# Kernel tuning notes

Measured on AMD Instinct MI355X. Metric: run time of the kernel, lower is better.

Reference implementation:

```python
import jax, jax.numpy as jnp
import numpy as np

N_NODES = 100_000
N_EDGES = 2_500_000
N_GRAPHS = 1000
F_IN, H, C = 4, 32, 3


def setup_inputs() -> dict:
    key = jax.random.key(0)
    ks = jax.random.split(key, 12)
    x = jax.random.normal(ks[0], (N_NODES, F_IN), dtype=jnp.float32)
    edge_index = jax.random.randint(ks[1], (2, N_EDGES), 0, N_NODES, dtype=jnp.int64)
    edge_weight = jax.random.uniform(ks[2], (N_EDGES,), dtype=jnp.float32)
    batch = jnp.sort(jax.random.randint(ks[3], (N_NODES,), 0, N_GRAPHS, dtype=jnp.int64))
    # GCNConv weights (glorot-ish) and biases
    W1 = jax.random.normal(ks[4], (F_IN, H), dtype=jnp.float32) * (1.0 / np.sqrt(F_IN))
    b1 = jnp.zeros((H,), dtype=jnp.float32)
    W2 = jax.random.normal(ks[5], (H, H), dtype=jnp.float32) * (1.0 / np.sqrt(H))
    b2 = jnp.zeros((H,), dtype=jnp.float32)
    W3 = jax.random.normal(ks[6], (H, H), dtype=jnp.float32) * (1.0 / np.sqrt(H))
    b3 = jnp.zeros((H,), dtype=jnp.float32)
    lin_w = jax.random.normal(ks[7], (H, C), dtype=jnp.float32) * (1.0 / np.sqrt(H))
    lin_b = jnp.zeros((C,), dtype=jnp.float32)
    return {"x": x, "edge_index": edge_index, "edge_weight": edge_weight, "batch": batch,
            "W1": W1, "b1": b1, "W2": W2, "b2": b2, "W3": W3, "b3": b3,
            "lin_w": lin_w, "lin_b": lin_b}


def _gcn_norm(edge_index, edge_weight, n_nodes):
    # PyG gcn_norm with add_self_loops=True: D^{-1/2} A_hat D^{-1/2}
    loop = jnp.arange(n_nodes, dtype=edge_index.dtype)
    row = jnp.concatenate([edge_index[0], loop])
    col = jnp.concatenate([edge_index[1], loop])
    w = jnp.concatenate([edge_weight, jnp.ones((n_nodes,), edge_weight.dtype)])
    deg = jax.ops.segment_sum(w, col, num_segments=n_nodes)
    dinv = jnp.where(deg > 0, jax.lax.rsqrt(jnp.where(deg > 0, deg, 1.0)), 0.0)
    norm = dinv[row] * w * dinv[col]
    return row, col, norm


def _gcn_conv(x, W, b, row, col, norm, n_nodes):
    h = x @ W                                  # [N, out]
    msg = norm[:, None] * h[row]               # gather + scale  [E+N, out]
    agg = jax.ops.segment_sum(msg, col, num_segments=n_nodes)
    return agg + b


def reference(x, edge_index, edge_weight, batch, W1, b1, W2, b2, W3, b3, lin_w, lin_b):
    n = x.shape[0]
    row, col, norm = _gcn_norm(edge_index, edge_weight, n)
    # dropout is identity in eval mode
    h = jax.nn.relu(_gcn_conv(x, W1, b1, row, col, norm, n))
    h = jax.nn.relu(_gcn_conv(h, W2, b2, row, col, norm, n))
    h = _gcn_conv(h, W3, b3, row, col, norm, n)
    # global_mean_pool over batch ids
    sums = jax.ops.segment_sum(h, batch, num_segments=N_GRAPHS)        # [G, H]
    cnt = jax.ops.segment_sum(jnp.ones((n,), h.dtype), batch, num_segments=N_GRAPHS)
    pooled = sums / jnp.maximum(cnt, 1.0)[:, None]
    return jax.nn.softmax(pooled @ lin_w + lin_b, axis=1)
```

## Files before the change

### kernel.cpp

```cpp
#include <hip/hip_runtime.h>
#include <hip/hip_fp16.h>

typedef unsigned long long ull;
typedef unsigned int uint;

#define BLOCK 256
#define CHUNK 8192
#define BN 128
#define PB 128
#define WINV (1.0f / 32768.0f)

__global__ void init_kernel(float* __restrict__ sums, float* __restrict__ cnt,
                            int* __restrict__ rowptr, int G, int nN, int nE) {
    int i = blockIdx.x * BLOCK + threadIdx.x;
    if (i < G * 32) sums[i] = 0.f;
    if (i < G) cnt[i] = 0.f;
    if (i == 0) rowptr[nN] = nE;
}

__global__ void p1_kernel(const int* __restrict__ col, int* __restrict__ cntmat,
                          int nE, int NBUK) {
    __shared__ int hist[1024];
    for (int i = threadIdx.x; i < NBUK; i += BLOCK) hist[i] = 0;
    __syncthreads();
    int base = blockIdx.x * CHUNK;
    int end = min(base + CHUNK, nE);
    for (int e = base + threadIdx.x; e < end; e += BLOCK)
        atomicAdd(&hist[col[e] >> 7], 1);
    __syncthreads();
    for (int i = threadIdx.x; i < NBUK; i += BLOCK)
        cntmat[(size_t)blockIdx.x * NBUK + i] = hist[i];
}

__global__ void p2a_kernel(int* __restrict__ cntmat, int* __restrict__ tot, int C, int NBUK) {
    int wv = threadIdx.x >> 6, lane = threadIdx.x & 63;
    int b = blockIdx.x * 4 + wv;
    if (b >= NBUK) return;
    int running = 0;
    for (int seg = 0; seg < C; seg += 64) {
        int c = seg + lane;
        int v = (c < C) ? cntmat[(size_t)c * NBUK + b] : 0;
        int s = v;
#pragma unroll
        for (int off = 1; off < 64; off <<= 1) {
            int u = __shfl_up(s, off);
            if (lane >= off) s += u;
        }
        if (c < C) cntmat[(size_t)c * NBUK + b] = running + (s - v);
        running += __shfl(s, 63);
    }
    if (lane == 0) tot[b] = running;
}

__global__ void p2b_kernel(const int* __restrict__ tot, int* __restrict__ bb, int NBUK, int nE) {
    __shared__ int s[1024];
    int t = threadIdx.x;
    int v = (t < NBUK) ? tot[t] : 0;
    s[t] = v;
    __syncthreads();
    for (int off = 1; off < 1024; off <<= 1) {
        int u = (t >= off) ? s[t - off] : 0;
        __syncthreads();
        s[t] += u;
        __syncthreads();
    }
    if (t < NBUK) bb[t] = s[t] - v;
    if (t == 0) bb[NBUK] = nE;
}

__global__ void p3_kernel(const int* __restrict__ row, const int* __restrict__ col,
                          const float* __restrict__ w, const int* __restrict__ cntmat,
                          const int* __restrict__ bb, ull* __restrict__ sorted,
                          int nE, int NBUK) {
    __shared__ int cur[1024];
    for (int i = threadIdx.x; i < NBUK; i += BLOCK)
        cur[i] = cntmat[(size_t)blockIdx.x * NBUK + i] + bb[i];
    __syncthreads();
    int base = blockIdx.x * CHUNK;
    int end = min(base + CHUNK, nE);
    for (int e = base + threadIdx.x; e < end; e += BLOCK) {
        int c = col[e], r = row[e];
        float ww = w[e];
        int b = c >> 7;
        int rk = atomicAdd(&cur[b], 1);
        ull ent = ((ull)(((uint)(c & 127) << 17) | (uint)r) << 32) | (ull)__float_as_uint(ww);
        sorted[rk] = ent;
    }
}

__global__ void p4_kernel(const ull* __restrict__ sorted, const int* __restrict__ bb,
                          float* __restrict__ dinv, int* __restrict__ rowptr,
                          uint* __restrict__ csr4, int nN) {
    __shared__ float wsum[BN];
    __shared__ int cntL[BN];
    __shared__ int scanS[BN];
    __shared__ int cur[BN];
    if (threadIdx.x < BN) { wsum[threadIdx.x] = 0.f; cntL[threadIdx.x] = 0; }
    __syncthreads();
    int b = blockIdx.x;
    int e0 = bb[b], e1 = bb[b + 1];
    for (int i = e0 + threadIdx.x; i < e1; i += BLOCK) {
        ull ent = sorted[i];
        int dl = (int)(ent >> 49) & 127;
        atomicAdd(&cntL[dl], 1);
        atomicAdd(&wsum[dl], __uint_as_float((uint)ent));
    }
    __syncthreads();
    if (threadIdx.x < BN) scanS[threadIdx.x] = cntL[threadIdx.x];
    __syncthreads();
    for (int off = 1; off < BN; off <<= 1) {
        int u = 0;
        if (threadIdx.x < BN && threadIdx.x >= off) u = scanS[threadIdx.x - off];
        __syncthreads();
        if (threadIdx.x < BN) scanS[threadIdx.x] += u;
        __syncthreads();
    }
    if (threadIdx.x < BN) {
        int n = b * BN + threadIdx.x;
        if (n < nN) {
            dinv[n] = rsqrtf(1.0f + wsum[threadIdx.x]);
            int rp = e0 + scanS[threadIdx.x] - cntL[threadIdx.x];
            rowptr[n] = rp;
            cur[threadIdx.x] = rp;
        }
    }
    __syncthreads();
    for (int i = e0 + threadIdx.x; i < e1; i += BLOCK) {
        ull ent = sorted[i];
        int dl = (int)(ent >> 49) & 127;
        uint src = (uint)(ent >> 32) & 0x1FFFFu;
        float ww = __uint_as_float((uint)ent);
        int wq = min((int)(ww * 32768.0f + 0.5f), 32767);
        int pos = atomicAdd(&cur[dl], 1);
        csr4[pos] = (src << 15) | (uint)wq;
    }
}

__global__ void ux_kernel(const float* __restrict__ x, const float* __restrict__ dinv,
                          float* __restrict__ u_x, int nN) {
    int i = blockIdx.x * BLOCK + threadIdx.x;
    if (i < nN * 4) u_x[i] = x[i] * dinv[i >> 2];
}

__global__ void layer1_pass(const float* __restrict__ u_x, const int* __restrict__ rowptr,
                            const uint* __restrict__ csr4, const float* __restrict__ dinv,
                            const float* __restrict__ W1, const float* __restrict__ b1,
                            const float* __restrict__ W2, __half* __restrict__ t_next, int nN) {
    __shared__ float W1s[4 * 32];
    __shared__ float W2s[32 * 32];
    __shared__ float b1s[32];
    __shared__ float hS[BLOCK / 64][32];
    if (threadIdx.x < 128) W1s[threadIdx.x] = W1[threadIdx.x];
    for (int i = threadIdx.x; i < 32 * 32; i += BLOCK) W2s[i] = W2[i];
    if (threadIdx.x < 32) b1s[threadIdx.x] = b1[threadIdx.x];
    __syncthreads();

    int wv = threadIdx.x >> 6, lane = threadIdx.x & 63;
    int n = blockIdx.x * (BLOCK / 64) + wv;
    if (n >= nN) return;

    int el = lane >> 2, comp = lane & 3;
    float di = dinv[n];
    int s0 = rowptr[n], s1 = rowptr[n + 1];
    float acc = (el == 0) ? u_x[(size_t)n * 4 + comp] : 0.0f;
    int j = s0;
    for (; j + 32 <= s1; j += 32) {
        uint ea = csr4[j + el], eb = csr4[j + 16 + el];
        acc = fmaf((float)(ea & 32767u) * WINV, u_x[(size_t)(ea >> 15) * 4 + comp], acc);
        acc = fmaf((float)(eb & 32767u) * WINV, u_x[(size_t)(eb >> 15) * 4 + comp], acc);
    }
    for (; j + 16 <= s1; j += 16) {
        uint e = csr4[j + el];
        acc = fmaf((float)(e & 32767u) * WINV, u_x[(size_t)(e >> 15) * 4 + comp], acc);
    }
    if (j + el < s1) {
        uint e = csr4[j + el];
        acc = fmaf((float)(e & 32767u) * WINV, u_x[(size_t)(e >> 15) * 4 + comp], acc);
    }
#pragma unroll
    for (int off = 4; off < 64; off <<= 1) acc += __shfl_xor(acc, off);
    float a0 = di * __shfl(acc, 0), a1 = di * __shfl(acc, 1);
    float a2c = di * __shfl(acc, 2), a3 = di * __shfl(acc, 3);

    int f = lane & 31, e2 = lane >> 5;
    float h = b1s[f];
    h = fmaf(a0, W1s[0 * 32 + f], h);
    h = fmaf(a1, W1s[1 * 32 + f], h);
    h = fmaf(a2c, W1s[2 * 32 + f], h);
    h = fmaf(a3, W1s[3 * 32 + f], h);
    h = fmaxf(h, 0.0f);
    if (lane < 32) hS[wv][f] = h;
    float o = 0.0f;
#pragma unroll
    for (int k = 0; k < 16; ++k) {
        int kk = e2 * 16 + k;
        o = fmaf(hS[wv][kk], W2s[kk * 32 + f], o);
    }
    o += __shfl_xor(o, 32);
    if (lane < 32) t_next[(size_t)n * 32 + f] = __float2half(di * o);
}

template <bool LAST>
__global__ void layer_pass(const __half* __restrict__ t, const int* __restrict__ rowptr,
                           const uint* __restrict__ csr4, const float* __restrict__ dinv,
                           const float* __restrict__ b, const float* __restrict__ W,
                           __half* __restrict__ t_next, __half* __restrict__ stage, int nN) {
    __shared__ float Ws[32 * 32];
    __shared__ float hS[BLOCK / 64][32];
    if (!LAST) {
        for (int i = threadIdx.x; i < 32 * 32; i += BLOCK) Ws[i] = W[i];
        __syncthreads();
    }
    int wv = threadIdx.x >> 6, lane = threadIdx.x & 63;
    int e2 = lane >> 5, f = lane & 31;
    int n = blockIdx.x * (BLOCK / 64) + wv;
    if (n >= nN) return;

    float di = dinv[n];
    int s0 = rowptr[n], s1 = rowptr[n + 1];
    float acc = (e2 == 0) ? __half2float(t[(size_t)n * 32 + f]) : 0.0f;

    int j4 = s0;
    for (; j4 + 16 <= s1; j4 += 16) {
        uint p[8]; float v[8];
#pragma unroll
        for (int u = 0; u < 8; ++u) p[u] = csr4[j4 + 2 * u + e2];
#pragma unroll
        for (int u = 0; u < 8; ++u) v[u] = __half2float(t[(size_t)(p[u] >> 15) * 32 + f]);
#pragma unroll
        for (int u = 0; u < 8; ++u) acc = fmaf((float)(p[u] & 32767u) * WINV, v[u], acc);
    }
    for (; j4 + 4 <= s1; j4 += 4) {
        uint p[2]; float v[2];
#pragma unroll
        for (int u = 0; u < 2; ++u) p[u] = csr4[j4 + 2 * u + e2];
#pragma unroll
        for (int u = 0; u < 2; ++u) v[u] = __half2float(t[(size_t)(p[u] >> 15) * 32 + f]);
#pragma unroll
        for (int u = 0; u < 2; ++u) acc = fmaf((float)(p[u] & 32767u) * WINV, v[u], acc);
    }
    for (int j = j4 + e2; j < s1; j += 2) {
        uint p = csr4[j];
        acc = fmaf((float)(p & 32767u) * WINV, __half2float(t[(size_t)(p >> 15) * 32 + f]), acc);
    }

    acc += __shfl_xor(acc, 32);
    float h = di * acc + b[f];

    if (LAST) {
        if (lane < 32) stage[(size_t)n * 32 + f] = __float2half(h);
    } else {
        h = fmaxf(h, 0.0f);
        if (lane < 32) hS[wv][f] = h;
        float o = 0.0f;
#pragma unroll
        for (int k = 0; k < 16; ++k) {
            int kk = e2 * 16 + k;
            o = fmaf(hS[wv][kk], Ws[kk * 32 + f], o);
        }
        o += __shfl_xor(o, 32);
        if (lane < 32) t_next[(size_t)n * 32 + f] = __float2half(di * o);
    }
}

__global__ void pool_kernel(const __half* __restrict__ stage, const int* __restrict__ batch,
                            float* __restrict__ sums, float* __restrict__ cnt, int nN) {
    __shared__ float accS[PB][32];
    __shared__ float cntS[PB];
    __shared__ int g0s;
    int n0 = blockIdx.x * PB;
    for (int i = threadIdx.x; i < PB * 32; i += BLOCK) ((float*)accS)[i] = 0.0f;
    for (int i = threadIdx.x; i < PB; i += BLOCK) cntS[i] = 0.0f;
    if (threadIdx.x == 0) g0s = batch[n0];
    __syncthreads();
    int g0 = g0s;
    int f = threadIdx.x & 31, sub = threadIdx.x >> 5;
    for (int k = 0; k < PB / 8; ++k) {
        int n = n0 + sub + k * 8;
        if (n < nN) {
            int g = batch[n];
            int off = g - g0;
            float v = __half2float(stage[(size_t)n * 32 + f]);
            if (off < PB) {
                atomicAdd(&accS[off][f], v);
                if (f == 0) atomicAdd(&cntS[off], 1.0f);
            } else {
                atomicAdd(&sums[(size_t)g * 32 + f], v);
                if (f == 0) atomicAdd(&cnt[g], 1.0f);
            }
        }
    }
    __syncthreads();
    int nLast = min(n0 + PB, nN) - 1;
    int range = min(batch[nLast] - g0, PB - 1);
    for (int s = sub; s <= range; s += 8) {
        atomicAdd(&sums[(size_t)(g0 + s) * 32 + f], accS[s][f]);
        if (f == 0) atomicAdd(&cnt[g0 + s], cntS[s]);
    }
}

__global__ void final_kernel(const float* __restrict__ sums, const float* __restrict__ cnt,
                             const float* __restrict__ lin_w, const float* __restrict__ lin_b,
                             float* __restrict__ out, int G) {
    int g = blockIdx.x * blockDim.x + threadIdx.x;
    if (g >= G) return;
    float c = fmaxf(cnt[g], 1.0f);
    float inv = 1.0f / c;
    float l0 = lin_b[0], l1 = lin_b[1], l2 = lin_b[2];
#pragma unroll
    for (int f = 0; f < 32; ++f) {
        float m = sums[g * 32 + f] * inv;
        l0 = fmaf(m, lin_w[f * 3 + 0], l0);
        l1 = fmaf(m, lin_w[f * 3 + 1], l1);
        l2 = fmaf(m, lin_w[f * 3 + 2], l2);
    }
    float mx = fmaxf(l0, fmaxf(l1, l2));
    float e0 = expf(l0 - mx), e1 = expf(l1 - mx), e2 = expf(l2 - mx);
    float s = 1.0f / (e0 + e1 + e2);
    out[g * 3 + 0] = e0 * s;
    out[g * 3 + 1] = e1 * s;
    out[g * 3 + 2] = e2 * s;
}


extern "C" void kernel_launch(void* const* d_in, const int* in_sizes, int n_in,
                              void* d_out, int out_size, void* d_ws, size_t ws_size,
                              hipStream_t stream) {
    const float* x     = (const float*)d_in[0];
    const int*   ei    = (const int*)d_in[1];
    const float* ew    = (const float*)d_in[2];
    const int*   batch = (const int*)d_in[3];
    const float* W1    = (const float*)d_in[4];
    const float* b1    = (const float*)d_in[5];
    const float* W2    = (const float*)d_in[6];
    const float* b2    = (const float*)d_in[7];
    const float* W3    = (const float*)d_in[8];
    const float* b3    = (const float*)d_in[9];
    const float* lin_w = (const float*)d_in[10];
    const float* lin_b = (const float*)d_in[11];
    float* out = (float*)d_out;

    const int nN = in_sizes[0] / 4;
    const int nE = in_sizes[2];
    const int G  = out_size / 3;
    const int* row = ei;
    const int* col = ei + nE;

    const int NBUK = (nN + BN - 1) / BN;
    const int C    = (nE + CHUNK - 1) / CHUNK;

    char* wsb = (char*)d_ws;
    ull*    sorted = (ull*)wsb;
    uint*   csr4   = (uint*)(sorted + nE);
    float*  u_x    = (float*)(csr4 + nE);
    __half* t_a    = (__half*)(u_x + (size_t)nN * 4);
    __half* t_b    = t_a + (size_t)nN * 32;
    __half* stage  = t_b + (size_t)nN * 32;
    int*    cntmat = (int*)(stage + (size_t)nN * 32);
    int*    tot    = cntmat + (size_t)C * NBUK;
    int*    bb     = tot + NBUK;
    float*  dinv   = (float*)(bb + NBUK + 1);
    int*    rowptr = (int*)(dinv + nN);
    float*  sums   = (float*)(rowptr + nN + 1);
    float*  cnt    = sums + (size_t)G * 32;

    const int gW = (nN + (BLOCK / 64) - 1) / (BLOCK / 64);

    init_kernel<<<(G * 32 + BLOCK - 1) / BLOCK, BLOCK, 0, stream>>>(sums, cnt, rowptr, G, nN, nE);
    p1_kernel<<<C, BLOCK, 0, stream>>>(col, cntmat, nE, NBUK);
    p2a_kernel<<<(NBUK + 3) / 4, BLOCK, 0, stream>>>(cntmat, tot, C, NBUK);
    p2b_kernel<<<1, 1024, 0, stream>>>(tot, bb, NBUK, nE);
    p3_kernel<<<C, BLOCK, 0, stream>>>(row, col, ew, cntmat, bb, sorted, nE, NBUK);
    p4_kernel<<<NBUK, BLOCK, 0, stream>>>(sorted, bb, dinv, rowptr, csr4, nN);
    ux_kernel<<<(nN * 4 + BLOCK - 1) / BLOCK, BLOCK, 0, stream>>>(x, dinv, u_x, nN);

    layer1_pass<<<gW, BLOCK, 0, stream>>>(u_x, rowptr, csr4, dinv, W1, b1, W2, t_b, nN);
    layer_pass<false><<<gW, BLOCK, 0, stream>>>(t_b, rowptr, csr4, dinv, b2, W3, t_a, nullptr, nN);
    layer_pass<true><<<gW, BLOCK, 0, stream>>>(t_a, rowptr, csr4, dinv, b3, nullptr, nullptr, stage, nN);

    pool_kernel<<<(nN + PB - 1) / PB, BLOCK, 0, stream>>>(stage, batch, sums, cnt, nN);
    final_kernel<<<(G + BLOCK - 1) / BLOCK, BLOCK, 0, stream>>>(sums, cnt, lin_w, lin_b, out, G);
}
```

Before: 377.0 us.

## Sort nodes by in-degree for load-balanced wavefront scheduling in GCN layers

Adds a counting sort of nodes by in-degree, capped at 63, built from a per-block histogram, a reuse of the existing scan kernels, and a scatter. The three layer passes then process nodes in this order through an indirection array. The goal is for wavefronts in the same block to handle nodes of similar degree, which cuts tail imbalance inside blocks. The cost is four extra launches, one extra indirect load per wave, and the loss of sequential node order, which hurts locality of dinv, rowptr and output writes.

```diff
diff --git a/kernel.cpp b/kernel.cpp
--- a/kernel.cpp
+++ b/kernel.cpp
@@ -52,7 +52,7 @@
     if (lane == 0) tot[b] = running;
 }
 
-__global__ void p2b_kernel(const int* __restrict__ tot, int* __restrict__ bb, int NBUK, int nE) {
+__global__ void p2b_kernel(const int* __restrict__ tot, int* __restrict__ bb, int NBUK, int total) {
     __shared__ int s[1024];
     int t = threadIdx.x;
     int v = (t < NBUK) ? tot[t] : 0;
@@ -65,7 +65,7 @@
         __syncthreads();
     }
     if (t < NBUK) bb[t] = s[t] - v;
-    if (t == 0) bb[NBUK] = nE;
+    if (t == 0) bb[NBUK] = total;
 }
 
 __global__ void p3_kernel(const int* __restrict__ row, const int* __restrict__ col,
@@ -136,6 +136,29 @@
     }
 }
 
+__global__ void q1_kernel(const int* __restrict__ rowptr, int* __restrict__ cntmatN, int nN) {
+    __shared__ int hist[64];
+    if (threadIdx.x < 64) hist[threadIdx.x] = 0;
+    __syncthreads();
+    int n = blockIdx.x * BLOCK + threadIdx.x;
+    if (n < nN) atomicAdd(&hist[min(rowptr[n + 1] - rowptr[n], 63)], 1);
+    __syncthreads();
+    if (threadIdx.x < 64) cntmatN[blockIdx.x * 64 + threadIdx.x] = hist[threadIdx.x];
+}
+
+__global__ void q3_kernel(const int* __restrict__ rowptr, const int* __restrict__ cntmatN,
+                          const int* __restrict__ bbN, int* __restrict__ order, int nN) {
+    __shared__ int cur[64];
+    if (threadIdx.x < 64)
+        cur[threadIdx.x] = cntmatN[blockIdx.x * 64 + threadIdx.x] + bbN[threadIdx.x];
+    __syncthreads();
+    int n = blockIdx.x * BLOCK + threadIdx.x;
+    if (n < nN) {
+        int rk = atomicAdd(&cur[min(rowptr[n + 1] - rowptr[n], 63)], 1);
+        order[rk] = n;
+    }
+}
+
 __global__ void ux_kernel(const float* __restrict__ x, const float* __restrict__ dinv,
                           float* __restrict__ u_x, int nN) {
     int i = blockIdx.x * BLOCK + threadIdx.x;
@@ -144,6 +167,7 @@
 
 __global__ void layer1_pass(const float* __restrict__ u_x, const int* __restrict__ rowptr,
                             const uint* __restrict__ csr4, const float* __restrict__ dinv,
+                            const int* __restrict__ order,
                             const float* __restrict__ W1, const float* __restrict__ b1,
                             const float* __restrict__ W2, __half* __restrict__ t_next, int nN) {
     __shared__ float W1s[4 * 32];
@@ -156,8 +180,9 @@
     __syncthreads();
 
     int wv = threadIdx.x >> 6, lane = threadIdx.x & 63;
-    int n = blockIdx.x * (BLOCK / 64) + wv;
-    if (n >= nN) return;
+    int widx = blockIdx.x * (BLOCK / 64) + wv;
+    if (widx >= nN) return;
+    int n = order[widx];
 
     int el = lane >> 2, comp = lane & 3;
     float di = dinv[n];
@@ -203,6 +228,7 @@
 template <bool LAST>
 __global__ void layer_pass(const __half* __restrict__ t, const int* __restrict__ rowptr,
                            const uint* __restrict__ csr4, const float* __restrict__ dinv,
+                           const int* __restrict__ order,
                            const float* __restrict__ b, const float* __restrict__ W,
                            __half* __restrict__ t_next, __half* __restrict__ stage, int nN) {
     __shared__ float Ws[32 * 32];
@@ -213,8 +239,9 @@
     }
     int wv = threadIdx.x >> 6, lane = threadIdx.x & 63;
     int e2 = lane >> 5, f = lane & 31;
-    int n = blockIdx.x * (BLOCK / 64) + wv;
-    if (n >= nN) return;
+    int widx = blockIdx.x * (BLOCK / 64) + wv;
+    if (widx >= nN) return;
+    int n = order[widx];
 
     float di = dinv[n];
     int s0 = rowptr[n], s1 = rowptr[n + 1];
@@ -348,6 +375,7 @@
 
     const int NBUK = (nN + BN - 1) / BN;
     const int C    = (nE + CHUNK - 1) / CHUNK;
+    const int NCN  = (nN + BLOCK - 1) / BLOCK;
 
     char* wsb = (char*)d_ws;
     ull*    sorted = (ull*)wsb;
@@ -361,7 +389,11 @@
     int*    bb     = tot + NBUK;
     float*  dinv   = (float*)(bb + NBUK + 1);
     int*    rowptr = (int*)(dinv + nN);
-    float*  sums   = (float*)(rowptr + nN + 1);
+    int*    order  = rowptr + nN + 1;
+    int*    cntmatN= order + nN;
+    int*    totN   = cntmatN + (size_t)NCN * 64;
+    int*    bbN    = totN + 64;
+    float*  sums   = (float*)(bbN + 65);
     float*  cnt    = sums + (size_t)G * 32;
 
     const int gW = (nN + (BLOCK / 64) - 1) / (BLOCK / 64);
@@ -374,9 +406,14 @@
     p4_kernel<<<NBUK, BLOCK, 0, stream>>>(sorted, bb, dinv, rowptr, csr4, nN);
     ux_kernel<<<(nN * 4 + BLOCK - 1) / BLOCK, BLOCK, 0, stream>>>(x, dinv, u_x, nN);
 
-    layer1_pass<<<gW, BLOCK, 0, stream>>>(u_x, rowptr, csr4, dinv, W1, b1, W2, t_b, nN);
-    layer_pass<false><<<gW, BLOCK, 0, stream>>>(t_b, rowptr, csr4, dinv, b2, W3, t_a, nullptr, nN);
-    layer_pass<true><<<gW, BLOCK, 0, stream>>>(t_a, rowptr, csr4, dinv, b3, nullptr, nullptr, stage, nN);
+    q1_kernel<<<NCN, BLOCK, 0, stream>>>(rowptr, cntmatN, nN);
+    p2a_kernel<<<16, BLOCK, 0, stream>>>(cntmatN, totN, NCN, 64);
+    p2b_kernel<<<1, 1024, 0, stream>>>(totN, bbN, 64, nN);
+    q3_kernel<<<NCN, BLOCK, 0, stream>>>(rowptr, cntmatN, bbN, order, nN);
+
+    layer1_pass<<<gW, BLOCK, 0, stream>>>(u_x, rowptr, csr4, dinv, order, W1, b1, W2, t_b, nN);
+    layer_pass<false><<<gW, BLOCK, 0, stream>>>(t_b, rowptr, csr4, dinv, order, b2, W3, t_a, nullptr, nN);
+    layer_pass<true><<<gW, BLOCK, 0, stream>>>(t_a, rowptr, csr4, dinv, order, b3, nullptr, nullptr, stage, nN);
 
     pool_kernel<<<(nN + PB - 1) / PB, BLOCK, 0, stream>>>(stage, batch, sums, cnt, nN);
     final_kernel<<<(G + BLOCK - 1) / BLOCK, BLOCK, 0, stream>>>(sums, cnt, lin_w, lin_b, out, G);
```

After: 385.9 us. +2.4%, slower.

## Shrink bucket-sort intermediates, pack degree atomics, fuse x scaling into CSR build

Applied to the files above, without the earlier changes.

The bucket-sort scatter now writes a 4-byte packed (source, quantized weight) word plus a 1-byte local destination, instead of an 8-byte entry. This cuts traffic through the sort intermediate. The CSR build kernel counts in-edges and sums quantized weights with a single packed 32-bit shared atomic. It also computes u_x = x*dinv directly, which removes the separate ux kernel. Each scatter block now handles two chunks. The degree sum now uses quantized weights, which changes precision slightly, and the 8-bit count field would overflow above 255 in-edges per node.

```diff
diff --git a/kernel.cpp b/kernel.cpp
--- a/kernel.cpp
+++ b/kernel.cpp
@@ -52,7 +52,7 @@
     if (lane == 0) tot[b] = running;
 }
 
-__global__ void p2b_kernel(const int* __restrict__ tot, int* __restrict__ bb, int NBUK, int nE) {
+__global__ void p2b_kernel(const int* __restrict__ tot, int* __restrict__ bb, int NBUK, int total) {
     __shared__ int s[1024];
     int t = threadIdx.x;
     int v = (t < NBUK) ? tot[t] : 0;
@@ -65,48 +65,47 @@
         __syncthreads();
     }
     if (t < NBUK) bb[t] = s[t] - v;
-    if (t == 0) bb[NBUK] = nE;
+    if (t == 0) bb[NBUK] = total;
 }
 
 __global__ void p3_kernel(const int* __restrict__ row, const int* __restrict__ col,
                           const float* __restrict__ w, const int* __restrict__ cntmat,
-                          const int* __restrict__ bb, ull* __restrict__ sorted,
-                          int nE, int NBUK) {
+                          const int* __restrict__ bb, uint* __restrict__ csrE,
+                          unsigned char* __restrict__ dl8, int nE, int NBUK) {
     __shared__ int cur[1024];
+    int c0 = blockIdx.x * 2;
     for (int i = threadIdx.x; i < NBUK; i += BLOCK)
-        cur[i] = cntmat[(size_t)blockIdx.x * NBUK + i] + bb[i];
-    __syncthreads();
-    int base = blockIdx.x * CHUNK;
-    int end = min(base + CHUNK, nE);
+        cur[i] = cntmat[(size_t)c0 * NBUK + i] + bb[i];
+    __syncthreads();
+    int base = c0 * CHUNK;
+    int end = min(base + 2 * CHUNK, nE);
     for (int e = base + threadIdx.x; e < end; e += BLOCK) {
         int c = col[e], r = row[e];
         float ww = w[e];
         int b = c >> 7;
-        int rk = atomicAdd(&cur[b], 1);
-        ull ent = ((ull)(((uint)(c & 127) << 17) | (uint)r) << 32) | (ull)__float_as_uint(ww);
-        sorted[rk] = ent;
-    }
-}
-
-__global__ void p4_kernel(const ull* __restrict__ sorted, const int* __restrict__ bb,
-                          float* __restrict__ dinv, int* __restrict__ rowptr,
-                          uint* __restrict__ csr4, int nN) {
-    __shared__ float wsum[BN];
-    __shared__ int cntL[BN];
+        int wq = min((int)(ww * 32768.0f + 0.5f), 32767);
+        int pos = atomicAdd(&cur[b], 1);
+        csrE[pos] = ((uint)r << 15) | (uint)wq;
+        dl8[pos] = (unsigned char)(c & 127);
+    }
+}
+
+__global__ void p4_kernel(const uint* __restrict__ csrE, const unsigned char* __restrict__ dl8,
+                          const int* __restrict__ bb, const float* __restrict__ x,
+                          float* __restrict__ u_x, float* __restrict__ dinv,
+                          int* __restrict__ rowptr, uint* __restrict__ csr4, int nN) {
+    __shared__ uint pk[BN];
     __shared__ int scanS[BN];
     __shared__ int cur[BN];
-    if (threadIdx.x < BN) { wsum[threadIdx.x] = 0.f; cntL[threadIdx.x] = 0; }
+    if (threadIdx.x < BN) pk[threadIdx.x] = 0u;
     __syncthreads();
     int b = blockIdx.x;
     int e0 = bb[b], e1 = bb[b + 1];
-    for (int i = e0 + threadIdx.x; i < e1; i += BLOCK) {
-        ull ent = sorted[i];
-        int dl = (int)(ent >> 49) & 127;
-        atomicAdd(&cntL[dl], 1);
-        atomicAdd(&wsum[dl], __uint_as_float((uint)ent));
-    }
-    __syncthreads();
-    if (threadIdx.x < BN) scanS[threadIdx.x] = cntL[threadIdx.x];
+    for (int i = e0 + threadIdx.x; i < e1; i += BLOCK)
+        atomicAdd(&pk[dl8[i]], (1u << 24) | (csrE[i] & 32767u));
+    __syncthreads();
+    int cnt = 0;
+    if (threadIdx.x < BN) { cnt = (int)(pk[threadIdx.x] >> 24); scanS[threadIdx.x] = cnt; }
     __syncthreads();
     for (int off = 1; off < BN; off <<= 1) {
         int u = 0;
@@ -118,28 +117,21 @@
     if (threadIdx.x < BN) {
         int n = b * BN + threadIdx.x;
         if (n < nN) {
-            dinv[n] = rsqrtf(1.0f + wsum[threadIdx.x]);
-            int rp = e0 + scanS[threadIdx.x] - cntL[threadIdx.x];
+            float di = rsqrtf(1.0f + (float)(pk[threadIdx.x] & 0xFFFFFFu) * WINV);
+            dinv[n] = di;
+            int rp = e0 + scanS[threadIdx.x] - cnt;
             rowptr[n] = rp;
             cur[threadIdx.x] = rp;
+            float4 xv = ((const float4*)x)[n];
+            ((float4*)u_x)[n] = make_float4(xv.x * di, xv.y * di, xv.z * di, xv.w * di);
         }
     }
     __syncthreads();
     for (int i = e0 + threadIdx.x; i < e1; i += BLOCK) {
-        ull ent = sorted[i];
-        int dl = (int)(ent >> 49) & 127;
-        uint src = (uint)(ent >> 32) & 0x1FFFFu;
-        float ww = __uint_as_float((uint)ent);
-        int wq = min((int)(ww * 32768.0f + 0.5f), 32767);
-        int pos = atomicAdd(&cur[dl], 1);
-        csr4[pos] = (src << 15) | (uint)wq;
-    }
-}
-
-__global__ void ux_kernel(const float* __restrict__ x, const float* __restrict__ dinv,
-                          float* __restrict__ u_x, int nN) {
-    int i = blockIdx.x * BLOCK + threadIdx.x;
-    if (i < nN * 4) u_x[i] = x[i] * dinv[i >> 2];
+        uint e = csrE[i];
+        int pos = atomicAdd(&cur[dl8[i]], 1);
+        csr4[pos] = e;
+    }
 }
 
 __global__ void layer1_pass(const float* __restrict__ u_x, const int* __restrict__ rowptr,
@@ -350,13 +342,14 @@
     const int C    = (nE + CHUNK - 1) / CHUNK;
 
     char* wsb = (char*)d_ws;
-    ull*    sorted = (ull*)wsb;
-    uint*   csr4   = (uint*)(sorted + nE);
+    uint*   csrE   = (uint*)wsb;
+    uint*   csr4   = csrE + nE;
     float*  u_x    = (float*)(csr4 + nE);
     __half* t_a    = (__half*)(u_x + (size_t)nN * 4);
     __half* t_b    = t_a + (size_t)nN * 32;
     __half* stage  = t_b + (size_t)nN * 32;
-    int*    cntmat = (int*)(stage + (size_t)nN * 32);
+    unsigned char* dl8 = (unsigned char*)(stage + (size_t)nN * 32);
+    int*    cntmat = (int*)(dl8 + nE);
     int*    tot    = cntmat + (size_t)C * NBUK;
     int*    bb     = tot + NBUK;
     float*  dinv   = (float*)(bb + NBUK + 1);
@@ -370,9 +363,8 @@
     p1_kernel<<<C, BLOCK, 0, stream>>>(col, cntmat, nE, NBUK);
     p2a_kernel<<<(NBUK + 3) / 4, BLOCK, 0, stream>>>(cntmat, tot, C, NBUK);
     p2b_kernel<<<1, 1024, 0, stream>>>(tot, bb, NBUK, nE);
-    p3_kernel<<<C, BLOCK, 0, stream>>>(row, col, ew, cntmat, bb, sorted, nE, NBUK);
-    p4_kernel<<<NBUK, BLOCK, 0, stream>>>(sorted, bb, dinv, rowptr, csr4, nN);
-    ux_kernel<<<(nN * 4 + BLOCK - 1) / BLOCK, BLOCK, 0, stream>>>(x, dinv, u_x, nN);
+    p3_kernel<<<(C + 1) / 2, BLOCK, 0, stream>>>(row, col, ew, cntmat, bb, csrE, dl8, nE, NBUK);
+    p4_kernel<<<NBUK, BLOCK, 0, stream>>>(csrE, dl8, bb, x, u_x, dinv, rowptr, csr4, nN);
 
     layer1_pass<<<gW, BLOCK, 0, stream>>>(u_x, rowptr, csr4, dinv, W1, b1, W2, t_b, nN);
     layer_pass<false><<<gW, BLOCK, 0, stream>>>(t_b, rowptr, csr4, dinv, b2, W3, t_a, nullptr, nN);
```

Measured after the change: 377.3 us. No clear change (+0.1%).

## Pack degree count and weight into one atomic, fuse ux into p4, halve chunk

Applied to the files above, without the earlier changes.

Edge weights are now quantised to 15 bits in p3, and each sorted entry packs the local destination, the source and the quantised weight. p4 then builds the degree count and the weight sum with a single integer shared atomic instead of an int atomic plus a float atomic, and writes csr4 by copying the low word. The separate ux_kernel is folded into p4 as a float4 scale of x by dinv. CHUNK is halved to give more blocks to the histogram and scatter passes, at the cost of a larger count matrix and scan. The degree is now computed from quantised weights, and the packed counter only holds up to 255 edges per node.

```diff
diff --git a/kernel.cpp b/kernel.cpp
--- a/kernel.cpp
+++ b/kernel.cpp
@@ -5,7 +5,7 @@
 typedef unsigned int uint;
 
 #define BLOCK 256
-#define CHUNK 8192
+#define CHUNK 4096
 #define BN 128
 #define PB 128
 #define WINV (1.0f / 32768.0f)
@@ -52,7 +52,7 @@
     if (lane == 0) tot[b] = running;
 }
 
-__global__ void p2b_kernel(const int* __restrict__ tot, int* __restrict__ bb, int NBUK, int nE) {
+__global__ void p2b_kernel(const int* __restrict__ tot, int* __restrict__ bb, int NBUK, int total) {
     __shared__ int s[1024];
     int t = threadIdx.x;
     int v = (t < NBUK) ? tot[t] : 0;
@@ -65,7 +65,7 @@
         __syncthreads();
     }
     if (t < NBUK) bb[t] = s[t] - v;
-    if (t == 0) bb[NBUK] = nE;
+    if (t == 0) bb[NBUK] = total;
 }
 
 __global__ void p3_kernel(const int* __restrict__ row, const int* __restrict__ col,
@@ -82,31 +82,30 @@
         int c = col[e], r = row[e];
         float ww = w[e];
         int b = c >> 7;
-        int rk = atomicAdd(&cur[b], 1);
-        ull ent = ((ull)(((uint)(c & 127) << 17) | (uint)r) << 32) | (ull)__float_as_uint(ww);
-        sorted[rk] = ent;
+        int wq = min((int)(ww * 32768.0f + 0.5f), 32767);
+        int pos = atomicAdd(&cur[b], 1);
+        sorted[pos] = ((ull)(uint)(c & 127) << 32) | ((ull)(uint)r << 15) | (ull)(uint)wq;
     }
 }
 
 __global__ void p4_kernel(const ull* __restrict__ sorted, const int* __restrict__ bb,
+                          const float* __restrict__ x, float* __restrict__ u_x,
                           float* __restrict__ dinv, int* __restrict__ rowptr,
                           uint* __restrict__ csr4, int nN) {
-    __shared__ float wsum[BN];
-    __shared__ int cntL[BN];
+    __shared__ uint pk[BN];
     __shared__ int scanS[BN];
     __shared__ int cur[BN];
-    if (threadIdx.x < BN) { wsum[threadIdx.x] = 0.f; cntL[threadIdx.x] = 0; }
+    if (threadIdx.x < BN) pk[threadIdx.x] = 0u;
     __syncthreads();
     int b = blockIdx.x;
     int e0 = bb[b], e1 = bb[b + 1];
     for (int i = e0 + threadIdx.x; i < e1; i += BLOCK) {
         ull ent = sorted[i];
-        int dl = (int)(ent >> 49) & 127;
-        atomicAdd(&cntL[dl], 1);
-        atomicAdd(&wsum[dl], __uint_as_float((uint)ent));
-    }
-    __syncthreads();
-    if (threadIdx.x < BN) scanS[threadIdx.x] = cntL[threadIdx.x];
+        atomicAdd(&pk[(int)(ent >> 32) & 127], (1u << 24) | ((uint)ent & 32767u));
+    }
+    __syncthreads();
+    int cnt = 0;
+    if (threadIdx.x < BN) { cnt = (int)(pk[threadIdx.x] >> 24); scanS[threadIdx.x] = cnt; }
     __syncthreads();
     for (int off = 1; off < BN; off <<= 1) {
         int u = 0;
@@ -118,28 +117,21 @@
     if (threadIdx.x < BN) {
         int n = b * BN + threadIdx.x;
         if (n < nN) {
-            dinv[n] = rsqrtf(1.0f + wsum[threadIdx.x]);
-            int rp = e0 + scanS[threadIdx.x] - cntL[threadIdx.x];
+            float di = rsqrtf(1.0f + (float)(pk[threadIdx.x] & 0xFFFFFFu) * WINV);
+            dinv[n] = di;
+            int rp = e0 + scanS[threadIdx.x] - cnt;
             rowptr[n] = rp;
             cur[threadIdx.x] = rp;
+            float4 xv = ((const float4*)x)[n];
+            ((float4*)u_x)[n] = make_float4(xv.x * di, xv.y * di, xv.z * di, xv.w * di);
         }
     }
     __syncthreads();
     for (int i = e0 + threadIdx.x; i < e1; i += BLOCK) {
         ull ent = sorted[i];
-        int dl = (int)(ent >> 49) & 127;
-        uint src = (uint)(ent >> 32) & 0x1FFFFu;
-        float ww = __uint_as_float((uint)ent);
-        int wq = min((int)(ww * 32768.0f + 0.5f), 32767);
-        int pos = atomicAdd(&cur[dl], 1);
-        csr4[pos] = (src << 15) | (uint)wq;
-    }
-}
-
-__global__ void ux_kernel(const float* __restrict__ x, const float* __restrict__ dinv,
-                          float* __restrict__ u_x, int nN) {
-    int i = blockIdx.x * BLOCK + threadIdx.x;
-    if (i < nN * 4) u_x[i] = x[i] * dinv[i >> 2];
+        int pos = atomicAdd(&cur[(int)(ent >> 32) & 127], 1);
+        csr4[pos] = (uint)ent;
+    }
 }
 
 __global__ void layer1_pass(const float* __restrict__ u_x, const int* __restrict__ rowptr,
@@ -371,8 +363,7 @@
     p2a_kernel<<<(NBUK + 3) / 4, BLOCK, 0, stream>>>(cntmat, tot, C, NBUK);
     p2b_kernel<<<1, 1024, 0, stream>>>(tot, bb, NBUK, nE);
     p3_kernel<<<C, BLOCK, 0, stream>>>(row, col, ew, cntmat, bb, sorted, nE, NBUK);
-    p4_kernel<<<NBUK, BLOCK, 0, stream>>>(sorted, bb, dinv, rowptr, csr4, nN);
-    ux_kernel<<<(nN * 4 + BLOCK - 1) / BLOCK, BLOCK, 0, stream>>>(x, dinv, u_x, nN);
+    p4_kernel<<<NBUK, BLOCK, 0, stream>>>(sorted, bb, x, u_x, dinv, rowptr, csr4, nN);
 
     layer1_pass<<<gW, BLOCK, 0, stream>>>(u_x, rowptr, csr4, dinv, W1, b1, W2, t_b, nN);
     layer_pass<false><<<gW, BLOCK, 0, stream>>>(t_b, rowptr, csr4, dinv, b2, W3, t_a, nullptr, nN);
```

New measurement: 352.0 us. 1.07x faster.
